# Optimization experiments

Measured on AMD Instinct MI355X. Metric: run time of the kernel, lower is better.

The kernel has to match this reference:

```python
import jax, jax.numpy as jnp
import numpy as np

B, T, I, H = 128, 512, 256, 256


def _gru_layer(x_seq, Wih, Whh, bih, bhh):
    """One GRU layer, batch_first. x_seq: [B, T, I_l]. Returns (outputs [B,T,H], h_T [B,H]).
    PyTorch gate order: r, z, n; n = tanh(Wn x + bn_i + r * (Un h + bn_h)); h' = (1-z)*n + z*h.
    """
    # Precompute input projections for all timesteps: [B, T, 3H]
    x_proj = jnp.einsum('bti,gi->btg', x_seq, Wih) + bih
    Wr_h, Wz_h, Wn_h = jnp.split(Whh, 3, axis=0)   # each [H, H]
    br_h, bz_h, bn_h = jnp.split(bhh, 3)

    def step(h, xp):  # h: [B, H], xp: [B, 3H]
        xr, xz, xn = jnp.split(xp, 3, axis=-1)
        r = jax.nn.sigmoid(xr + h @ Wr_h.T + br_h)
        z = jax.nn.sigmoid(xz + h @ Wz_h.T + bz_h)
        n = jnp.tanh(xn + r * (h @ Wn_h.T + bn_h))
        h_new = (1.0 - z) * n + z * h
        return h_new, h_new

    h0 = jnp.zeros((x_seq.shape[0], Whh.shape[1]), dtype=x_seq.dtype)
    hT, outs = jax.lax.scan(step, h0, jnp.swapaxes(x_proj, 0, 1))  # scan over time
    return jnp.swapaxes(outs, 0, 1), hT


def setup_inputs() -> dict:
    key = jax.random.key(0)
    ks = jax.random.split(key, 12)
    s = 1.0 / np.sqrt(H)  # torch GRU/Linear init scale
    u = lambda k, shape: jax.random.uniform(k, shape, jnp.float32, -s, s)
    return {
        'x': jax.random.normal(ks[0], (B, T, I), jnp.float32),
        'Wih0': u(ks[1], (3 * H, I)),
        'Whh0': u(ks[2], (3 * H, H)),
        'bih0': u(ks[3], (3 * H,)),
        'bhh0': u(ks[4], (3 * H,)),
        'Wih1': u(ks[5], (3 * H, H)),
        'Whh1': u(ks[6], (3 * H, H)),
        'bih1': u(ks[7], (3 * H,)),
        'bhh1': u(ks[8], (3 * H,)),
        'Wfc': u(ks[9], (1, H)),
        'bfc': u(ks[10], (1,)),
    }


def reference(x, Wih0, Whh0, bih0, bhh0, Wih1, Whh1, bih1, bhh1, Wfc, bfc):
    out0, _ = _gru_layer(x, Wih0, Whh0, bih0, bhh0)      # layer 0 outputs [B,T,H]
    _, hT1 = _gru_layer(out0, Wih1, Whh1, bih1, bhh1)     # final hidden of layer 1 [B,H]
    y_logit = hT1 @ Wfc.T + bfc                            # [B, 1]
    return jax.nn.sigmoid(y_logit)
```

## Files before the change

### kernel.cpp

```cpp
#include <hip/hip_runtime.h>
#include <hip/hip_bf16.h>
#include <stdint.h>

#define NB 128
#define NT 512
#define NI 256
#define NH 256
#define NG 768

typedef unsigned int u32;
typedef unsigned short u16;
typedef __attribute__((ext_vector_type(8))) short short8;
typedef __attribute__((ext_vector_type(4))) float f32x4;

__device__ __forceinline__ float lo_bf(u32 u){ return __uint_as_float(u << 16); }
__device__ __forceinline__ float hi_bf(u32 u){ return __uint_as_float(u & 0xffff0000u); }
__device__ __forceinline__ u16 f2bf(float f){
  u32 u = __float_as_uint(f);
  u += 0x7fffu + ((u >> 16) & 1u);
  return (u16)(u >> 16);
}
__device__ __forceinline__ u32 pack2(float a, float b){
  return (u32)f2bf(a) | ((u32)f2bf(b) << 16);
}
__device__ __forceinline__ u32 pack_rne(float a, float b){
  u32 ua = __float_as_uint(a), ub = __float_as_uint(b);
  ua += 0x7fffu + ((ua >> 16) & 1u);
  ub += 0x7fffu + ((ub >> 16) & 1u);
  return (ua >> 16) | (ub & 0xffff0000u);
}
__device__ __forceinline__ float sigf(float v){
  return __builtin_amdgcn_rcpf(1.f + __expf(-v));
}
__device__ __forceinline__ float tanhf_(float u){
  float e = __expf(2.f*u);
  return 1.f - 2.f*__builtin_amdgcn_rcpf(e + 1.f);
}
__device__ __forceinline__ void gload_lds16(const void* g, void* l){
  __builtin_amdgcn_global_load_lds((const __attribute__((address_space(1))) void*)g,
                                   (__attribute__((address_space(3))) void*)l, 16, 0, 0);
}

__global__ void convert_kernel(const float* __restrict__ x,
    const float* __restrict__ Wih0, const float* __restrict__ Wih1,
    const float* __restrict__ bih0, const float* __restrict__ bhh0,
    const float* __restrict__ bih1, const float* __restrict__ bhh1,
    u16* __restrict__ xbf, u16* __restrict__ w0bf, u16* __restrict__ w1bf,
    float* __restrict__ bias0, float* __restrict__ bias1)
{
  const int NX4 = NB*NT*NI/4, NW4 = NG*NH/4;
  int gid = blockIdx.x*blockDim.x + threadIdx.x;
  for (int i = gid; i < NX4 + 2*NW4; i += gridDim.x*blockDim.x) {
    const float* s; u16* d; int o;
    if (i < NX4)          { s = x;    d = xbf;  o = i; }
    else if (i < NX4+NW4) { s = Wih0; d = w0bf; o = i - NX4; }
    else                  { s = Wih1; d = w1bf; o = i - NX4 - NW4; }
    float4 v = *(const float4*)(s + (size_t)o*4);
    uint2 pk; pk.x = pack2(v.x, v.y); pk.y = pack2(v.z, v.w);
    *(uint2*)&d[(size_t)o*4] = pk;
  }
  if (gid < NG)            bias0[gid] = bih0[gid] + (gid < 2*NH ? bhh0[gid] : 0.f);
  else if (gid < 2*NG)   { int g = gid - NG; bias1[g] = bih1[g] + (g < 2*NH ? bhh1[g] : 0.f); }
}

__global__ __launch_bounds__(256, 2) void gemm_proj(const u16* __restrict__ A,
    const u16* __restrict__ W, const float* __restrict__ bias, u16* __restrict__ out)
{
  const int mt = blockIdx.x / 24, nt = blockIdx.x % 24;
  __shared__ __align__(16) u16 As[64*256];
  __shared__ __align__(16) u16 Bs[32*256];
  const int tid = threadIdx.x;
  const u16* Ag = A + (size_t)mt*64*256;
  const u16* Wg = W + (size_t)nt*32*256;
  #pragma unroll
  for (int i = 0; i < 8; ++i) {
    int ca = tid + 256*i, row = ca >> 5, sl = ca & 31;
    gload_lds16(Ag + row*256 + ((sl ^ (row&7))<<3), &As[ca<<3]);
  }
  #pragma unroll
  for (int i = 0; i < 4; ++i) {
    int cb = tid + 256*i, row = cb >> 5, sl = cb & 31;
    gload_lds16(Wg + row*256 + ((sl ^ (row&7))<<3), &Bs[cb<<3]);
  }
  __syncthreads();
  const int w = tid >> 6, l = tid & 63, c = l & 15, q = l >> 4;
  f32x4 acc0 = {0.f,0.f,0.f,0.f}, acc1 = acc0;
  const int arow = w*16 + c;
  #pragma unroll
  for (int kb = 0; kb < 8; ++kb) {
    int ks = kb*4 + q;
    short8 af  = *(const short8*)&As[arow*256 + ((ks ^ (arow&7))<<3)];
    short8 bf0 = *(const short8*)&Bs[c*256        + ((ks ^ (c&7))<<3)];
    short8 bf1 = *(const short8*)&Bs[(16+c)*256   + ((ks ^ ((16+c)&7))<<3)];
    acc0 = __builtin_amdgcn_mfma_f32_16x16x32_bf16(af, bf0, acc0, 0,0,0);
    acc1 = __builtin_amdgcn_mfma_f32_16x16x32_bf16(af, bf1, acc1, 0,0,0);
  }
  #pragma unroll
  for (int nf = 0; nf < 2; ++nf) {
    int g = nt*32 + nf*16 + c;
    float bs = bias[g];
    f32x4 av = nf ? acc1 : acc0;
    #pragma unroll
    for (int r = 0; r < 4; ++r) {
      int m = mt*64 + w*16 + q*4 + r;
      out[(size_t)m*NG + g] = f2bf(av[r] + bs);
    }
  }
}

__global__ __launch_bounds__(512, 1) void recur_kernel(
    const u16* __restrict__ xproj,
    const float* __restrict__ Whh,
    const float* __restrict__ bhh,
    u16* __restrict__ outp,
    int write_all)
{
  const int b0 = blockIdx.x * 8;
  const int tid = threadIdx.x;
  const int w = tid >> 6, l = tid & 63, c = l & 15, q = l >> 4;
  const int jh = c >> 3;
  const bool lo8 = (jh == 0);
  const int bb = b0 + (c & 7);
  const int jb = 32*w + jh*16 + q*4;

  __shared__ __align__(16) u16 hfrag[2][8][512];
  for (int i = tid; i < 4096; i += 512) ((u32*)hfrag)[i] = 0u;

  short8 wf[3][2][8];
  #pragma unroll
  for (int g = 0; g < 3; ++g)
    #pragma unroll
    for (int jj = 0; jj < 2; ++jj) {
      const float* src = Whh + ((size_t)(g*NH + 32*w + jj*16 + c))*NI + q*8;
      #pragma unroll
      for (int kb = 0; kb < 8; ++kb) {
        float4 f0 = *(const float4*)(src + kb*32);
        float4 f1 = *(const float4*)(src + kb*32 + 4);
        short8 s;
        s[0]=(short)f2bf(f0.x); s[1]=(short)f2bf(f0.y);
        s[2]=(short)f2bf(f0.z); s[3]=(short)f2bf(f0.w);
        s[4]=(short)f2bf(f1.x); s[5]=(short)f2bf(f1.y);
        s[6]=(short)f2bf(f1.z); s[7]=(short)f2bf(f1.w);
        wf[g][jj][kb] = s;
      }
    }

  float4 bt0 = *(const float4*)&bhh[2*NH + 32*w + q*4];
  float4 bt1 = *(const float4*)&bhh[2*NH + 32*w + q*4 + 16];
  f32x4 bhn0; bhn0[0]=bt0.x; bhn0[1]=bt0.y; bhn0[2]=bt0.z; bhn0[3]=bt0.w;
  f32x4 bhn1; bhn1[0]=bt1.x; bhn1[1]=bt1.y; bhn1[2]=bt1.z; bhn1[3]=bt1.w;

  const u16* xptr = xproj + (size_t)bb*NT*NG + jb;
  uint2 xpr = *(const uint2*)(xptr);
  uint2 xpz = *(const uint2*)(xptr + NH);
  uint2 xpn = *(const uint2*)(xptr + 2*NH);
  uint2 hpk; hpk.x = 0u; hpk.y = 0u;

  const int lp = (c & 7) + 16*(2*jh + (q >> 1));
  __syncthreads();

  #pragma unroll 1
  for (int t = 0; t < NT; ++t) {
    const int cur = t & 1, nxt = cur ^ 1;

    short8 bfr[8];
    #pragma unroll
    for (int kb = 0; kb < 8; ++kb) bfr[kb] = *(const short8*)&hfrag[cur][kb][l*8];

    const u16* xnx = xptr + (size_t)((t+1 < NT) ? t+1 : t)*NG;
    uint2 nxr = *(const uint2*)(xnx);
    uint2 nxz = *(const uint2*)(xnx + NH);
    uint2 nxn = *(const uint2*)(xnx + 2*NH);

    f32x4 z4 = {0.f,0.f,0.f,0.f};
    f32x4 ar0 = z4, az0 = z4, ar1 = z4, az1 = z4;
    f32x4 an0 = bhn0, an1 = bhn1;
    #pragma unroll
    for (int kb = 0; kb < 8; ++kb) {
      short8 bv = bfr[kb];
      ar0 = __builtin_amdgcn_mfma_f32_16x16x32_bf16(wf[0][0][kb], bv, ar0, 0,0,0);
      az0 = __builtin_amdgcn_mfma_f32_16x16x32_bf16(wf[1][0][kb], bv, az0, 0,0,0);
      an0 = __builtin_amdgcn_mfma_f32_16x16x32_bf16(wf[2][0][kb], bv, an0, 0,0,0);
      ar1 = __builtin_amdgcn_mfma_f32_16x16x32_bf16(wf[0][1][kb], bv, ar1, 0,0,0);
      az1 = __builtin_amdgcn_mfma_f32_16x16x32_bf16(wf[1][1][kb], bv, az1, 0,0,0);
      an1 = __builtin_amdgcn_mfma_f32_16x16x32_bf16(wf[2][1][kb], bv, an1, 0,0,0);
    }

    float hv[4];
    #pragma unroll
    for (int r = 0; r < 4; ++r) {
      float arv = lo8 ? ar0[r] : ar1[r];
      float azv = lo8 ? az0[r] : az1[r];
      float anv = lo8 ? an0[r] : an1[r];
      u32 xrw = (r < 2) ? xpr.x : xpr.y;
      u32 xzw = (r < 2) ? xpz.x : xpz.y;
      u32 xnw = (r < 2) ? xpn.x : xpn.y;
      u32 hpw = (r < 2) ? hpk.x : hpk.y;
      float xr = (r & 1) ? hi_bf(xrw) : lo_bf(xrw);
      float xz = (r & 1) ? hi_bf(xzw) : lo_bf(xzw);
      float xn = (r & 1) ? hi_bf(xnw) : lo_bf(xnw);
      float hp = (r & 1) ? hi_bf(hpw) : lo_bf(hpw);
      float rr = sigf(xr + arv);
      float zz = sigf(xz + azv);
      float nn = tanhf_(__builtin_fmaf(rr, anv, xn));
      hv[r] = __builtin_fmaf(zz, hp - nn, nn);
    }
    hpk.x = pack_rne(hv[0], hv[1]);
    hpk.y = pack_rne(hv[2], hv[3]);

    u16* hdst = &hfrag[nxt][w][lp*8 + (q & 1)*4];
    *(uint2*)hdst        = hpk;
    *(uint2*)(hdst + 64) = hpk;
    if (write_all)
      *(uint2*)&outp[((size_t)bb*NT + t)*NH + jb] = hpk;
    else if (t == NT-1)
      *(uint2*)&outp[(size_t)bb*NH + jb] = hpk;

    xpr = nxr; xpz = nxz; xpn = nxn;
    __syncthreads();
  }
}

__global__ __launch_bounds__(256) void fc_kernel(const u16* __restrict__ hT,
    const float* __restrict__ Wfc, const float* __restrict__ bfc, float* __restrict__ out)
{
  __shared__ float wv[NH];
  int tid = threadIdx.x;
  if (tid < NH) wv[tid] = Wfc[tid];
  __syncthreads();
  if (tid < NB) {
    float acc = bfc[0];
    for (int j = 0; j < NH; ++j) acc += lo_bf((u32)hT[tid*NH + j]) * wv[j];
    out[tid] = sigf(acc);
  }
}

extern "C" void kernel_launch(void* const* d_in, const int* in_sizes, int n_in,
                              void* d_out, int out_size, void* d_ws, size_t ws_size,
                              hipStream_t stream) {
  const float* x    = (const float*)d_in[0];
  const float* Wih0 = (const float*)d_in[1];
  const float* Whh0 = (const float*)d_in[2];
  const float* bih0 = (const float*)d_in[3];
  const float* bhh0 = (const float*)d_in[4];
  const float* Wih1 = (const float*)d_in[5];
  const float* Whh1 = (const float*)d_in[6];
  const float* bih1 = (const float*)d_in[7];
  const float* bhh1 = (const float*)d_in[8];
  const float* Wfc  = (const float*)d_in[9];
  const float* bfc  = (const float*)d_in[10];

  char* ws = (char*)d_ws;
  u16*   xproj = (u16*)ws;
  u16*   xbf   = (u16*)(ws + 100663296);
  u16*   out0  = xbf;
  u16*   w0bf  = (u16*)(ws + 134217728);
  u16*   w1bf  = (u16*)(ws + 134610944);
  float* bias0 = (float*)(ws + 135004160);
  float* bias1 = (float*)(ws + 135007232);
  u16*   hT    = (u16*)(ws + 135010304);

  convert_kernel<<<dim3(2048), dim3(256), 0, stream>>>(
      x, Wih0, Wih1, bih0, bhh0, bih1, bhh1, xbf, w0bf, w1bf, bias0, bias1);
  gemm_proj<<<dim3(1024*24), dim3(256), 0, stream>>>(xbf, w0bf, bias0, xproj);
  recur_kernel<<<dim3(16), dim3(512), 0, stream>>>(xproj, Whh0, bhh0, out0, 1);
  gemm_proj<<<dim3(1024*24), dim3(256), 0, stream>>>(out0, w1bf, bias1, xproj);
  recur_kernel<<<dim3(16), dim3(512), 0, stream>>>(xproj, Whh1, bhh1, hT, 0);
  fc_kernel<<<dim3(1), dim3(256), 0, stream>>>(hT, Wfc, bfc, (float*)d_out);
}
```

Before: 1.399 ms.

## Pipeline both GRU layers and layer-1 input projection in one persistent kernel

Replaces the sequential layer-0 recurrence, layer-1 projection GEMM and layer-1 recurrence with one 48-block kernel split into three roles per batch group. The roles stream results through ring-buffer FIFOs in global memory, using agent-scope atomic counters for flow control. The aim is to overlap the two recurrences in a wavefront pipeline, so the second serial 512-step loop mostly hides behind the first. It also drops the full out0 write and the second large GEMM. The cost is spin-wait synchronisation latency on every step, a dependence on all 48 blocks being co-resident, and a per-timestep Wih1 matvec done on only 16 blocks.

```diff
diff --git a/kernel.cpp b/kernel.cpp
--- a/kernel.cpp
+++ b/kernel.cpp
@@ -7,8 +7,11 @@
 #define NI 256
 #define NH 256
 #define NG 768
+#define NGRP 16
+#define RING 32
 
 typedef unsigned int u32;
+typedef unsigned long long u64;
 typedef unsigned short u16;
 typedef __attribute__((ext_vector_type(8))) short short8;
 typedef __attribute__((ext_vector_type(4))) float f32x4;
@@ -29,6 +32,10 @@
   ub += 0x7fffu + ((ub >> 16) & 1u);
   return (ua >> 16) | (ub & 0xffff0000u);
 }
+__device__ __forceinline__ u64 pack4(const f32x4& v){
+  u32 a = pack_rne(v[0], v[1]), b = pack_rne(v[2], v[3]);
+  return (u64)a | ((u64)b << 32);
+}
 __device__ __forceinline__ float sigf(float v){
   return __builtin_amdgcn_rcpf(1.f + __expf(-v));
 }
@@ -40,27 +47,57 @@
   __builtin_amdgcn_global_load_lds((const __attribute__((address_space(1))) void*)g,
                                    (__attribute__((address_space(3))) void*)l, 16, 0, 0);
 }
+__device__ __forceinline__ void st_agent(u64* p, u64 v){
+  __hip_atomic_store(p, v, __ATOMIC_RELAXED, __HIP_MEMORY_SCOPE_AGENT);
+}
+__device__ __forceinline__ u64 ld_agent(const u64* p){
+  return __hip_atomic_load(p, __ATOMIC_RELAXED, __HIP_MEMORY_SCOPE_AGENT);
+}
+__device__ __forceinline__ u32 spin_ge(u32* p, u32 target, u32 shadow){
+  while (shadow < target) {
+    shadow = __hip_atomic_load(p, __ATOMIC_ACQUIRE, __HIP_MEMORY_SCOPE_AGENT);
+    if (shadow >= target) break;
+    __builtin_amdgcn_s_sleep(2);
+  }
+  return shadow;
+}
+__device__ __forceinline__ void load_frags(const float* W, int w, int c, int q,
+                                           short8 wf[3][2][8]){
+  #pragma unroll
+  for (int g = 0; g < 3; ++g)
+    #pragma unroll
+    for (int jj = 0; jj < 2; ++jj) {
+      const float* src = W + ((size_t)(g*NH + 32*w + jj*16 + c))*NI + q*8;
+      #pragma unroll
+      for (int kb = 0; kb < 8; ++kb) {
+        float4 f0 = *(const float4*)(src + kb*32);
+        float4 f1 = *(const float4*)(src + kb*32 + 4);
+        short8 s;
+        s[0]=(short)f2bf(f0.x); s[1]=(short)f2bf(f0.y);
+        s[2]=(short)f2bf(f0.z); s[3]=(short)f2bf(f0.w);
+        s[4]=(short)f2bf(f1.x); s[5]=(short)f2bf(f1.y);
+        s[6]=(short)f2bf(f1.z); s[7]=(short)f2bf(f1.w);
+        wf[g][jj][kb] = s;
+      }
+    }
+}
 
 __global__ void convert_kernel(const float* __restrict__ x,
-    const float* __restrict__ Wih0, const float* __restrict__ Wih1,
+    const float* __restrict__ Wih0,
     const float* __restrict__ bih0, const float* __restrict__ bhh0,
-    const float* __restrict__ bih1, const float* __restrict__ bhh1,
-    u16* __restrict__ xbf, u16* __restrict__ w0bf, u16* __restrict__ w1bf,
-    float* __restrict__ bias0, float* __restrict__ bias1)
+    u16* __restrict__ xbf, u16* __restrict__ w0bf, float* __restrict__ bias0)
 {
   const int NX4 = NB*NT*NI/4, NW4 = NG*NH/4;
   int gid = blockIdx.x*blockDim.x + threadIdx.x;
-  for (int i = gid; i < NX4 + 2*NW4; i += gridDim.x*blockDim.x) {
+  for (int i = gid; i < NX4 + NW4; i += gridDim.x*blockDim.x) {
     const float* s; u16* d; int o;
-    if (i < NX4)          { s = x;    d = xbf;  o = i; }
-    else if (i < NX4+NW4) { s = Wih0; d = w0bf; o = i - NX4; }
-    else                  { s = Wih1; d = w1bf; o = i - NX4 - NW4; }
+    if (i < NX4) { s = x;    d = xbf;  o = i; }
+    else         { s = Wih0; d = w0bf; o = i - NX4; }
     float4 v = *(const float4*)(s + (size_t)o*4);
     uint2 pk; pk.x = pack2(v.x, v.y); pk.y = pack2(v.z, v.w);
     *(uint2*)&d[(size_t)o*4] = pk;
   }
-  if (gid < NG)            bias0[gid] = bih0[gid] + (gid < 2*NH ? bhh0[gid] : 0.f);
-  else if (gid < 2*NG)   { int g = gid - NG; bias1[g] = bih1[g] + (g < 2*NH ? bhh1[g] : 0.f); }
+  if (gid < NG) bias0[gid] = bih0[gid] + (gid < 2*NH ? bhh0[gid] : 0.f);
 }
 
 __global__ __launch_bounds__(256, 2) void gemm_proj(const u16* __restrict__ A,
@@ -108,116 +145,284 @@
   }
 }
 
-__global__ __launch_bounds__(512, 1) void recur_kernel(
-    const u16* __restrict__ xproj,
-    const float* __restrict__ Whh,
-    const float* __restrict__ bhh,
-    u16* __restrict__ outp,
-    int write_all)
+__global__ __launch_bounds__(512, 1) void pipeline_kernel(
+    const u16*  __restrict__ xproj,
+    const float* __restrict__ Whh0, const float* __restrict__ bhh0,
+    const float* __restrict__ Wih1, const float* __restrict__ bih1,
+    const float* __restrict__ bhh1, const float* __restrict__ Whh1,
+    u16* __restrict__ hT,
+    u16* __restrict__ fifo_h0,
+    u16* __restrict__ fifo_xp,
+    u32* __restrict__ cnts)
 {
-  const int b0 = blockIdx.x * 8;
+  const int role = blockIdx.x >> 4;
+  const int g_   = blockIdx.x & 15;
+  const int b0   = g_*8;
   const int tid = threadIdx.x;
   const int w = tid >> 6, l = tid & 63, c = l & 15, q = l >> 4;
-  const int jh = c >> 3;
-  const bool lo8 = (jh == 0);
-  const int bb = b0 + (c & 7);
-  const int jb = 32*w + jh*16 + q*4;
+
+  u32* cntA = cnts + (0*NGRP + g_)*32;
+  u32* cntB = cnts + (1*NGRP + g_)*32;
+  u32* cntC = cnts + (2*NGRP + g_)*32;
+  u16* slots_h0 = fifo_h0 + (size_t)g_*RING*4096;
+  u16* slots_xp = fifo_xp + (size_t)g_*RING*8*NG;
 
   __shared__ __align__(16) u16 hfrag[2][8][512];
   for (int i = tid; i < 4096; i += 512) ((u32*)hfrag)[i] = 0u;
-
-  short8 wf[3][2][8];
-  #pragma unroll
-  for (int g = 0; g < 3; ++g)
+  __syncthreads();
+
+  if (role == 0) {
+    short8 wf[3][2][8];
+    load_frags(Whh0, w, c, q, wf);
+    float4 bt0 = *(const float4*)&bhh0[2*NH + 32*w + q*4];
+    float4 bt1 = *(const float4*)&bhh0[2*NH + 32*w + q*4 + 16];
+    f32x4 bhn0; bhn0[0]=bt0.x; bhn0[1]=bt0.y; bhn0[2]=bt0.z; bhn0[3]=bt0.w;
+    f32x4 bhn1; bhn1[0]=bt1.x; bhn1[1]=bt1.y; bhn1[2]=bt1.z; bhn1[3]=bt1.w;
+    const int jh = c >> 3;
+    const bool lo8 = (jh == 0);
+    const int bb = b0 + (c & 7);
+    const int jb = 32*w + jh*16 + q*4;
+    const u16* xptr = xproj + (size_t)bb*NT*NG + jb;
+    uint2 xpr = *(const uint2*)(xptr);
+    uint2 xpz = *(const uint2*)(xptr + NH);
+    uint2 xpn = *(const uint2*)(xptr + 2*NH);
+    const u16* x1 = xptr + NG;
+    uint2 pfr = *(const uint2*)(x1);
+    uint2 pfz = *(const uint2*)(x1 + NH);
+    uint2 pfn = *(const uint2*)(x1 + 2*NH);
+    uint2 hpk; hpk.x = 0u; hpk.y = 0u;
+    const int lp = (c&7) + 16*(2*jh + (q>>1));
+    const int foff = w*512 + lp*8 + (q&1)*4;
+    u32 shadowB = 0;
+
+    #pragma unroll 1
+    for (int t = 0; t < NT; ++t) {
+      const int cur = t & 1, nxt = cur ^ 1;
+      short8 bfr[8];
+      #pragma unroll
+      for (int kb = 0; kb < 8; ++kb) bfr[kb] = *(const short8*)&hfrag[cur][kb][l*8];
+      f32x4 z4 = {0.f,0.f,0.f,0.f};
+      f32x4 ar0 = z4, az0 = z4, ar1 = z4, az1 = z4;
+      f32x4 an0 = bhn0, an1 = bhn1;
+      #pragma unroll
+      for (int kb = 0; kb < 8; ++kb) {
+        short8 bv = bfr[kb];
+        ar0 = __builtin_amdgcn_mfma_f32_16x16x32_bf16(wf[0][0][kb], bv, ar0, 0,0,0);
+        az0 = __builtin_amdgcn_mfma_f32_16x16x32_bf16(wf[1][0][kb], bv, az0, 0,0,0);
+        an0 = __builtin_amdgcn_mfma_f32_16x16x32_bf16(wf[2][0][kb], bv, an0, 0,0,0);
+        ar1 = __builtin_amdgcn_mfma_f32_16x16x32_bf16(wf[0][1][kb], bv, ar1, 0,0,0);
+        az1 = __builtin_amdgcn_mfma_f32_16x16x32_bf16(wf[1][1][kb], bv, az1, 0,0,0);
+        an1 = __builtin_amdgcn_mfma_f32_16x16x32_bf16(wf[2][1][kb], bv, an1, 0,0,0);
+      }
+      float hv[4];
+      #pragma unroll
+      for (int r = 0; r < 4; ++r) {
+        float arv = lo8 ? ar0[r] : ar1[r];
+        float azv = lo8 ? az0[r] : az1[r];
+        float anv = lo8 ? an0[r] : an1[r];
+        u32 xrw = (r < 2) ? xpr.x : xpr.y;
+        u32 xzw = (r < 2) ? xpz.x : xpz.y;
+        u32 xnw = (r < 2) ? xpn.x : xpn.y;
+        u32 hpw = (r < 2) ? hpk.x : hpk.y;
+        float xr = (r & 1) ? hi_bf(xrw) : lo_bf(xrw);
+        float xz = (r & 1) ? hi_bf(xzw) : lo_bf(xzw);
+        float xn = (r & 1) ? hi_bf(xnw) : lo_bf(xnw);
+        float hp = (r & 1) ? hi_bf(hpw) : lo_bf(hpw);
+        float rr = sigf(xr + arv);
+        float zz = sigf(xz + azv);
+        float nn = tanhf_(__builtin_fmaf(rr, anv, xn));
+        hv[r] = __builtin_fmaf(zz, hp - nn, nn);
+      }
+      hpk.x = pack_rne(hv[0], hv[1]);
+      hpk.y = pack_rne(hv[2], hv[3]);
+
+      u16* hdst = &hfrag[nxt][w][lp*8 + (q&1)*4];
+      *(uint2*)hdst        = hpk;
+      *(uint2*)(hdst + 64) = hpk;
+
+      if (t >= 29) {
+        u32 tgt = 8u*(u32)(t - 28);
+        if (shadowB < tgt) shadowB = spin_ge(cntB, tgt, shadowB);
+      }
+      u64 hv64 = (u64)hpk.x | ((u64)hpk.y << 32);
+      u16* sb = slots_h0 + (size_t)(t & (RING-1))*4096 + foff;
+      st_agent((u64*)sb, hv64);
+      st_agent((u64*)(sb + 64), hv64);
+      if (l == 0)
+        __hip_atomic_fetch_add(cntA, 1u, __ATOMIC_RELEASE, __HIP_MEMORY_SCOPE_AGENT);
+
+      xpr = pfr; xpz = pfz; xpn = pfn;
+      if (t + 2 < NT) {
+        const u16* xn_ = xptr + (size_t)(t+2)*NG;
+        pfr = *(const uint2*)(xn_);
+        pfz = *(const uint2*)(xn_ + NH);
+        pfn = *(const uint2*)(xn_ + 2*NH);
+      }
+      asm volatile("s_waitcnt lgkmcnt(0)" ::: "memory");
+      __builtin_amdgcn_s_barrier();
+      __builtin_amdgcn_sched_barrier(0);
+    }
+
+  } else if (role == 1) {
+    short8 wf[3][2][8];
+    load_frags(Wih1, w, c, q, wf);
+    f32x4 bias[3][2];
     #pragma unroll
-    for (int jj = 0; jj < 2; ++jj) {
-      const float* src = Whh + ((size_t)(g*NH + 32*w + jj*16 + c))*NI + q*8;
+    for (int g = 0; g < 3; ++g)
+      #pragma unroll
+      for (int jj = 0; jj < 2; ++jj) {
+        int grow = g*NH + 32*w + jj*16 + q*4;
+        float4 bi = *(const float4*)&bih1[grow];
+        f32x4 bv; bv[0]=bi.x; bv[1]=bi.y; bv[2]=bi.z; bv[3]=bi.w;
+        if (g < 2) {
+          float4 bh = *(const float4*)&bhh1[grow];
+          bv[0]+=bh.x; bv[1]+=bh.y; bv[2]+=bh.z; bv[3]+=bh.w;
+        }
+        bias[g][jj] = bv;
+      }
+    const int jj = c >> 3;
+    u32 shadowA = 0, shadowC = 0;
+    shadowA = spin_ge(cntA, 8u, shadowA);
+    const u16* s0 = slots_h0 + 0*4096 + tid*8;
+    u64 wc0 = ld_agent((const u64*)s0), wc1 = ld_agent((const u64*)(s0 + 4));
+    shadowA = spin_ge(cntA, 16u, shadowA);
+    const u16* s1 = slots_h0 + 1*4096 + tid*8;
+    u64 pf0 = ld_agent((const u64*)s1), pf1 = ld_agent((const u64*)(s1 + 4));
+
+    #pragma unroll 1
+    for (int t = 0; t < NT; ++t) {
+      const int buf = t & 1;
+      uint4 wv; wv.x=(u32)wc0; wv.y=(u32)(wc0>>32); wv.z=(u32)wc1; wv.w=(u32)(wc1>>32);
+      *(uint4*)&((u16*)hfrag)[buf*4096 + tid*8] = wv;
+      asm volatile("s_waitcnt lgkmcnt(0)" ::: "memory");
+      __builtin_amdgcn_s_barrier();
+      __builtin_amdgcn_sched_barrier(0);
+
+      f32x4 a00 = bias[0][0], a10 = bias[1][0], a20 = bias[2][0];
+      f32x4 a01 = bias[0][1], a11 = bias[1][1], a21 = bias[2][1];
       #pragma unroll
       for (int kb = 0; kb < 8; ++kb) {
-        float4 f0 = *(const float4*)(src + kb*32);
-        float4 f1 = *(const float4*)(src + kb*32 + 4);
-        short8 s;
-        s[0]=(short)f2bf(f0.x); s[1]=(short)f2bf(f0.y);
-        s[2]=(short)f2bf(f0.z); s[3]=(short)f2bf(f0.w);
-        s[4]=(short)f2bf(f1.x); s[5]=(short)f2bf(f1.y);
-        s[6]=(short)f2bf(f1.z); s[7]=(short)f2bf(f1.w);
-        wf[g][jj][kb] = s;
+        short8 bv = *(const short8*)&hfrag[buf][kb][l*8];
+        a00 = __builtin_amdgcn_mfma_f32_16x16x32_bf16(wf[0][0][kb], bv, a00, 0,0,0);
+        a10 = __builtin_amdgcn_mfma_f32_16x16x32_bf16(wf[1][0][kb], bv, a10, 0,0,0);
+        a20 = __builtin_amdgcn_mfma_f32_16x16x32_bf16(wf[2][0][kb], bv, a20, 0,0,0);
+        a01 = __builtin_amdgcn_mfma_f32_16x16x32_bf16(wf[0][1][kb], bv, a01, 0,0,0);
+        a11 = __builtin_amdgcn_mfma_f32_16x16x32_bf16(wf[1][1][kb], bv, a11, 0,0,0);
+        a21 = __builtin_amdgcn_mfma_f32_16x16x32_bf16(wf[2][1][kb], bv, a21, 0,0,0);
+      }
+      f32x4 v0 = jj ? a01 : a00, v1 = jj ? a11 : a10, v2 = jj ? a21 : a20;
+      if (t >= 29) {
+        u32 tgt = 8u*(u32)(t - 28);
+        if (shadowC < tgt) shadowC = spin_ge(cntC, tgt, shadowC);
+      }
+      u16* xb_ = slots_xp + (size_t)(t & (RING-1))*8*NG
+               + (size_t)(c & 7)*NG + 32*w + jj*16 + q*4;
+      st_agent((u64*)(xb_),        pack4(v0));
+      st_agent((u64*)(xb_ + NH),   pack4(v1));
+      st_agent((u64*)(xb_ + 2*NH), pack4(v2));
+      if (l == 0)
+        __hip_atomic_fetch_add(cntB, 1u, __ATOMIC_RELEASE, __HIP_MEMORY_SCOPE_AGENT);
+      wc0 = pf0; wc1 = pf1;
+      if (t + 2 < NT) {
+        u32 tgt = 8u*(u32)(t + 3);
+        if (shadowA < tgt) shadowA = spin_ge(cntA, tgt, shadowA);
+        const u16* sn = slots_h0 + (size_t)((t+2) & (RING-1))*4096 + tid*8;
+        pf0 = ld_agent((const u64*)sn); pf1 = ld_agent((const u64*)(sn + 4));
       }
     }
 
-  float4 bt0 = *(const float4*)&bhh[2*NH + 32*w + q*4];
-  float4 bt1 = *(const float4*)&bhh[2*NH + 32*w + q*4 + 16];
-  f32x4 bhn0; bhn0[0]=bt0.x; bhn0[1]=bt0.y; bhn0[2]=bt0.z; bhn0[3]=bt0.w;
-  f32x4 bhn1; bhn1[0]=bt1.x; bhn1[1]=bt1.y; bhn1[2]=bt1.z; bhn1[3]=bt1.w;
-
-  const u16* xptr = xproj + (size_t)bb*NT*NG + jb;
-  uint2 xpr = *(const uint2*)(xptr);
-  uint2 xpz = *(const uint2*)(xptr + NH);
-  uint2 xpn = *(const uint2*)(xptr + 2*NH);
-  uint2 hpk; hpk.x = 0u; hpk.y = 0u;
-
-  const int lp = (c & 7) + 16*(2*jh + (q >> 1));
-  __syncthreads();
-
-  #pragma unroll 1
-  for (int t = 0; t < NT; ++t) {
-    const int cur = t & 1, nxt = cur ^ 1;
-
-    short8 bfr[8];
-    #pragma unroll
-    for (int kb = 0; kb < 8; ++kb) bfr[kb] = *(const short8*)&hfrag[cur][kb][l*8];
-
-    const u16* xnx = xptr + (size_t)((t+1 < NT) ? t+1 : t)*NG;
-    uint2 nxr = *(const uint2*)(xnx);
-    uint2 nxz = *(const uint2*)(xnx + NH);
-    uint2 nxn = *(const uint2*)(xnx + 2*NH);
-
-    f32x4 z4 = {0.f,0.f,0.f,0.f};
-    f32x4 ar0 = z4, az0 = z4, ar1 = z4, az1 = z4;
-    f32x4 an0 = bhn0, an1 = bhn1;
-    #pragma unroll
-    for (int kb = 0; kb < 8; ++kb) {
-      short8 bv = bfr[kb];
-      ar0 = __builtin_amdgcn_mfma_f32_16x16x32_bf16(wf[0][0][kb], bv, ar0, 0,0,0);
-      az0 = __builtin_amdgcn_mfma_f32_16x16x32_bf16(wf[1][0][kb], bv, az0, 0,0,0);
-      an0 = __builtin_amdgcn_mfma_f32_16x16x32_bf16(wf[2][0][kb], bv, an0, 0,0,0);
-      ar1 = __builtin_amdgcn_mfma_f32_16x16x32_bf16(wf[0][1][kb], bv, ar1, 0,0,0);
-      az1 = __builtin_amdgcn_mfma_f32_16x16x32_bf16(wf[1][1][kb], bv, az1, 0,0,0);
-      an1 = __builtin_amdgcn_mfma_f32_16x16x32_bf16(wf[2][1][kb], bv, an1, 0,0,0);
+  } else {
+    short8 wf[3][2][8];
+    load_frags(Whh1, w, c, q, wf);
+    float4 bt0 = *(const float4*)&bhh1[2*NH + 32*w + q*4];
+    float4 bt1 = *(const float4*)&bhh1[2*NH + 32*w + q*4 + 16];
+    f32x4 bhn0; bhn0[0]=bt0.x; bhn0[1]=bt0.y; bhn0[2]=bt0.z; bhn0[3]=bt0.w;
+    f32x4 bhn1; bhn1[0]=bt1.x; bhn1[1]=bt1.y; bhn1[2]=bt1.z; bhn1[3]=bt1.w;
+    const int jh = c >> 3;
+    const bool lo8 = (jh == 0);
+    const int bb = b0 + (c & 7);
+    const int jb = 32*w + jh*16 + q*4;
+    const int lp = (c&7) + 16*(2*jh + (q>>1));
+    const size_t xoff = (size_t)(c & 7)*NG + jb;
+    u32 shadowB = 0;
+    shadowB = spin_ge(cntB, 8u, shadowB);
+    u64 vr = ld_agent((const u64*)(slots_xp + xoff));
+    u64 vz = ld_agent((const u64*)(slots_xp + xoff + NH));
+    u64 vn = ld_agent((const u64*)(slots_xp + xoff + 2*NH));
+    uint2 xpr, xpz, xpn;
+    xpr.x=(u32)vr; xpr.y=(u32)(vr>>32);
+    xpz.x=(u32)vz; xpz.y=(u32)(vz>>32);
+    xpn.x=(u32)vn; xpn.y=(u32)(vn>>32);
+    shadowB = spin_ge(cntB, 16u, shadowB);
+    u64 pr = ld_agent((const u64*)(slots_xp + 1*8*NG + xoff));
+    u64 pz = ld_agent((const u64*)(slots_xp + 1*8*NG + xoff + NH));
+    u64 pn = ld_agent((const u64*)(slots_xp + 1*8*NG + xoff + 2*NH));
+    uint2 hpk; hpk.x = 0u; hpk.y = 0u;
+
+    #pragma unroll 1
+    for (int t = 0; t < NT; ++t) {
+      const int cur = t & 1, nxt = cur ^ 1;
+      short8 bfr[8];
+      #pragma unroll
+      for (int kb = 0; kb < 8; ++kb) bfr[kb] = *(const short8*)&hfrag[cur][kb][l*8];
+      f32x4 z4 = {0.f,0.f,0.f,0.f};
+      f32x4 ar0 = z4, az0 = z4, ar1 = z4, az1 = z4;
+      f32x4 an0 = bhn0, an1 = bhn1;
+      #pragma unroll
+      for (int kb = 0; kb < 8; ++kb) {
+        short8 bv = bfr[kb];
+        ar0 = __builtin_amdgcn_mfma_f32_16x16x32_bf16(wf[0][0][kb], bv, ar0, 0,0,0);
+        az0 = __builtin_amdgcn_mfma_f32_16x16x32_bf16(wf[1][0][kb], bv, az0, 0,0,0);
+        an0 = __builtin_amdgcn_mfma_f32_16x16x32_bf16(wf[2][0][kb], bv, an0, 0,0,0);
+        ar1 = __builtin_amdgcn_mfma_f32_16x16x32_bf16(wf[0][1][kb], bv, ar1, 0,0,0);
+        az1 = __builtin_amdgcn_mfma_f32_16x16x32_bf16(wf[1][1][kb], bv, az1, 0,0,0);
+        an1 = __builtin_amdgcn_mfma_f32_16x16x32_bf16(wf[2][1][kb], bv, an1, 0,0,0);
+      }
+      float hv[4];
+      #pragma unroll
+      for (int r = 0; r < 4; ++r) {
+        float arv = lo8 ? ar0[r] : ar1[r];
+        float azv = lo8 ? az0[r] : az1[r];
+        float anv = lo8 ? an0[r] : an1[r];
+        u32 xrw = (r < 2) ? xpr.x : xpr.y;
+        u32 xzw = (r < 2) ? xpz.x : xpz.y;
+        u32 xnw = (r < 2) ? xpn.x : xpn.y;
+        u32 hpw = (r < 2) ? hpk.x : hpk.y;
+        float xr = (r & 1) ? hi_bf(xrw) : lo_bf(xrw);
+        float xz = (r & 1) ? hi_bf(xzw) : lo_bf(xzw);
+        float xn = (r & 1) ? hi_bf(xnw) : lo_bf(xnw);
+        float hp = (r & 1) ? hi_bf(hpw) : lo_bf(hpw);
+        float rr = sigf(xr + arv);
+        float zz = sigf(xz + azv);
+        float nn = tanhf_(__builtin_fmaf(rr, anv, xn));
+        hv[r] = __builtin_fmaf(zz, hp - nn, nn);
+      }
+      hpk.x = pack_rne(hv[0], hv[1]);
+      hpk.y = pack_rne(hv[2], hv[3]);
+
+      u16* hdst = &hfrag[nxt][w][lp*8 + (q&1)*4];
+      *(uint2*)hdst        = hpk;
+      *(uint2*)(hdst + 64) = hpk;
+      if (t == NT-1)
+        *(uint2*)&hT[(size_t)bb*NH + jb] = hpk;
+      if (l == 0)
+        __hip_atomic_fetch_add(cntC, 1u, __ATOMIC_RELEASE, __HIP_MEMORY_SCOPE_AGENT);
+
+      xpr.x=(u32)pr; xpr.y=(u32)(pr>>32);
+      xpz.x=(u32)pz; xpz.y=(u32)(pz>>32);
+      xpn.x=(u32)pn; xpn.y=(u32)(pn>>32);
+      if (t + 2 < NT) {
+        u32 tgt = 8u*(u32)(t + 3);
+        if (shadowB < tgt) shadowB = spin_ge(cntB, tgt, shadowB);
+        const u16* sn = slots_xp + (size_t)((t+2) & (RING-1))*8*NG + xoff;
+        pr = ld_agent((const u64*)(sn));
+        pz = ld_agent((const u64*)(sn + NH));
+        pn = ld_agent((const u64*)(sn + 2*NH));
+      }
+      asm volatile("s_waitcnt lgkmcnt(0)" ::: "memory");
+      __builtin_amdgcn_s_barrier();
+      __builtin_amdgcn_sched_barrier(0);
     }
-
-    float hv[4];
-    #pragma unroll
-    for (int r = 0; r < 4; ++r) {
-      float arv = lo8 ? ar0[r] : ar1[r];
-      float azv = lo8 ? az0[r] : az1[r];
-      float anv = lo8 ? an0[r] : an1[r];
-      u32 xrw = (r < 2) ? xpr.x : xpr.y;
-      u32 xzw = (r < 2) ? xpz.x : xpz.y;
-      u32 xnw = (r < 2) ? xpn.x : xpn.y;
-      u32 hpw = (r < 2) ? hpk.x : hpk.y;
-      float xr = (r & 1) ? hi_bf(xrw) : lo_bf(xrw);
-      float xz = (r & 1) ? hi_bf(xzw) : lo_bf(xzw);
-      float xn = (r & 1) ? hi_bf(xnw) : lo_bf(xnw);
-      float hp = (r & 1) ? hi_bf(hpw) : lo_bf(hpw);
-      float rr = sigf(xr + arv);
-      float zz = sigf(xz + azv);
-      float nn = tanhf_(__builtin_fmaf(rr, anv, xn));
-      hv[r] = __builtin_fmaf(zz, hp - nn, nn);
-    }
-    hpk.x = pack_rne(hv[0], hv[1]);
-    hpk.y = pack_rne(hv[2], hv[3]);
-
-    u16* hdst = &hfrag[nxt][w][lp*8 + (q & 1)*4];
-    *(uint2*)hdst        = hpk;
-    *(uint2*)(hdst + 64) = hpk;
-    if (write_all)
-      *(uint2*)&outp[((size_t)bb*NT + t)*NH + jb] = hpk;
-    else if (t == NT-1)
-      *(uint2*)&outp[(size_t)bb*NH + jb] = hpk;
-
-    xpr = nxr; xpz = nxz; xpn = nxn;
-    __syncthreads();
   }
 }
 
@@ -251,20 +456,20 @@
   const float* bfc  = (const float*)d_in[10];
 
   char* ws = (char*)d_ws;
-  u16*   xproj = (u16*)ws;
-  u16*   xbf   = (u16*)(ws + 100663296);
-  u16*   out0  = xbf;
-  u16*   w0bf  = (u16*)(ws + 134217728);
-  u16*   w1bf  = (u16*)(ws + 134610944);
-  float* bias0 = (float*)(ws + 135004160);
-  float* bias1 = (float*)(ws + 135007232);
-  u16*   hT    = (u16*)(ws + 135010304);
+  u16*   xproj   = (u16*)ws;
+  u16*   xbf     = (u16*)(ws + 100663296);
+  u16*   fifo_h0 = (u16*)(ws + 100663296);
+  u16*   fifo_xp = (u16*)(ws + 100663296 + 4194304);
+  u32*   cnts    = (u32*)(ws + 100663296 + 4194304 + 6291456);
+  u16*   w0bf    = (u16*)(ws + 134217728);
+  float* bias0   = (float*)(ws + 135004160);
+  u16*   hT      = (u16*)(ws + 135010304);
 
   convert_kernel<<<dim3(2048), dim3(256), 0, stream>>>(
-      x, Wih0, Wih1, bih0, bhh0, bih1, bhh1, xbf, w0bf, w1bf, bias0, bias1);
+      x, Wih0, bih0, bhh0, xbf, w0bf, bias0);
   gemm_proj<<<dim3(1024*24), dim3(256), 0, stream>>>(xbf, w0bf, bias0, xproj);
-  recur_kernel<<<dim3(16), dim3(512), 0, stream>>>(xproj, Whh0, bhh0, out0, 1);
-  gemm_proj<<<dim3(1024*24), dim3(256), 0, stream>>>(out0, w1bf, bias1, xproj);
-  recur_kernel<<<dim3(16), dim3(512), 0, stream>>>(xproj, Whh1, bhh1, hT, 0);
+  hipMemsetAsync(cnts, 0, 3*NGRP*32*sizeof(u32), stream);
+  pipeline_kernel<<<dim3(48), dim3(512), 0, stream>>>(
+      xproj, Whh0, bhh0, Wih1, bih1, bhh1, Whh1, hT, fifo_h0, fifo_xp, cnts);
   fc_kernel<<<dim3(1), dim3(256), 0, stream>>>(hT, Wfc, bfc, (float*)d_out);
 }
```

New measurement: 3.318 ms. +137.1%, slower.

## Split recurrence over twice as many blocks with four batch rows each

Applied to the files above, without the earlier changes.

Each recurrent block now handles 4 batch rows instead of 8, so the grid doubles from 16 to 32 blocks and each lane finishes 2 hidden outputs instead of 4. The hidden-state fragment is replicated four times in LDS to fill the 16-wide MFMA column dimension, so half the MFMA columns do redundant work. The input-projection prefetch now runs two steps ahead. Priority is raised around the MFMA loop, and the per-step __syncthreads is replaced by an explicit lgkm wait plus a raw barrier. The aim is to shorten the serial per-step elementwise tail and use more CUs, at the cost of wasted matrix throughput.

```diff
diff --git a/kernel.cpp b/kernel.cpp
--- a/kernel.cpp
+++ b/kernel.cpp
@@ -115,13 +115,15 @@
     u16* __restrict__ outp,
     int write_all)
 {
-  const int b0 = blockIdx.x * 8;
+  const int b0 = blockIdx.x * 4;
   const int tid = threadIdx.x;
   const int w = tid >> 6, l = tid & 63, c = l & 15, q = l >> 4;
   const int jh = c >> 3;
+  const int rs = (c >> 2) & 1;
   const bool lo8 = (jh == 0);
-  const int bb = b0 + (c & 7);
-  const int jb = 32*w + jh*16 + q*4;
+  const bool rlo = (rs == 0);
+  const int bb = b0 + (c & 3);
+  const int j0 = 32*w + jh*16 + q*4 + 2*rs;
 
   __shared__ __align__(16) u16 hfrag[2][8][512];
   for (int i = tid; i < 4096; i += 512) ((u32*)hfrag)[i] = 0u;
@@ -150,13 +152,20 @@
   f32x4 bhn0; bhn0[0]=bt0.x; bhn0[1]=bt0.y; bhn0[2]=bt0.z; bhn0[3]=bt0.w;
   f32x4 bhn1; bhn1[0]=bt1.x; bhn1[1]=bt1.y; bhn1[2]=bt1.z; bhn1[3]=bt1.w;
 
-  const u16* xptr = xproj + (size_t)bb*NT*NG + jb;
-  uint2 xpr = *(const uint2*)(xptr);
-  uint2 xpz = *(const uint2*)(xptr + NH);
-  uint2 xpn = *(const uint2*)(xptr + 2*NH);
-  uint2 hpk; hpk.x = 0u; hpk.y = 0u;
-
-  const int lp = (c & 7) + 16*(2*jh + (q >> 1));
+  const u16* xptr = xproj + (size_t)bb*NT*NG + j0;
+  u32 xpr = *(const u32*)(xptr);
+  u32 xpz = *(const u32*)(xptr + NH);
+  u32 xpn = *(const u32*)(xptr + 2*NH);
+  const u16* x1 = xptr + NG;
+  u32 pfr = *(const u32*)(x1);
+  u32 pfz = *(const u32*)(x1 + NH);
+  u32 pfn = *(const u32*)(x1 + 2*NH);
+  u32 hpk = 0u;
+
+  const int lpb  = (c & 3) + 16*(2*jh + (q >> 1));
+  const int elds = 4*(q & 1) + 2*rs;
+  const int woff = lpb*8 + elds;
+
   __syncthreads();
 
   #pragma unroll 1
@@ -167,14 +176,10 @@
     #pragma unroll
     for (int kb = 0; kb < 8; ++kb) bfr[kb] = *(const short8*)&hfrag[cur][kb][l*8];
 
-    const u16* xnx = xptr + (size_t)((t+1 < NT) ? t+1 : t)*NG;
-    uint2 nxr = *(const uint2*)(xnx);
-    uint2 nxz = *(const uint2*)(xnx + NH);
-    uint2 nxn = *(const uint2*)(xnx + 2*NH);
-
     f32x4 z4 = {0.f,0.f,0.f,0.f};
     f32x4 ar0 = z4, az0 = z4, ar1 = z4, az1 = z4;
     f32x4 an0 = bhn0, an1 = bhn1;
+    __builtin_amdgcn_s_setprio(1);
     #pragma unroll
     for (int kb = 0; kb < 8; ++kb) {
       short8 bv = bfr[kb];
@@ -185,39 +190,53 @@
       az1 = __builtin_amdgcn_mfma_f32_16x16x32_bf16(wf[1][1][kb], bv, az1, 0,0,0);
       an1 = __builtin_amdgcn_mfma_f32_16x16x32_bf16(wf[2][1][kb], bv, an1, 0,0,0);
     }
-
-    float hv[4];
-    #pragma unroll
-    for (int r = 0; r < 4; ++r) {
-      float arv = lo8 ? ar0[r] : ar1[r];
-      float azv = lo8 ? az0[r] : az1[r];
-      float anv = lo8 ? an0[r] : an1[r];
-      u32 xrw = (r < 2) ? xpr.x : xpr.y;
-      u32 xzw = (r < 2) ? xpz.x : xpz.y;
-      u32 xnw = (r < 2) ? xpn.x : xpn.y;
-      u32 hpw = (r < 2) ? hpk.x : hpk.y;
-      float xr = (r & 1) ? hi_bf(xrw) : lo_bf(xrw);
-      float xz = (r & 1) ? hi_bf(xzw) : lo_bf(xzw);
-      float xn = (r & 1) ? hi_bf(xnw) : lo_bf(xnw);
-      float hp = (r & 1) ? hi_bf(hpw) : lo_bf(hpw);
+    __builtin_amdgcn_s_setprio(0);
+
+    float hv[2];
+    #pragma unroll
+    for (int e = 0; e < 2; ++e) {
+      float a0 = rlo ? ar0[e] : ar0[2+e];
+      float a1 = rlo ? ar1[e] : ar1[2+e];
+      float arv = lo8 ? a0 : a1;
+      float z0 = rlo ? az0[e] : az0[2+e];
+      float z1 = rlo ? az1[e] : az1[2+e];
+      float azv = lo8 ? z0 : z1;
+      float n0 = rlo ? an0[e] : an0[2+e];
+      float n1 = rlo ? an1[e] : an1[2+e];
+      float anv = lo8 ? n0 : n1;
+      float xr = e ? hi_bf(xpr) : lo_bf(xpr);
+      float xz = e ? hi_bf(xpz) : lo_bf(xpz);
+      float xn = e ? hi_bf(xpn) : lo_bf(xpn);
+      float hp = e ? hi_bf(hpk) : lo_bf(hpk);
       float rr = sigf(xr + arv);
       float zz = sigf(xz + azv);
       float nn = tanhf_(__builtin_fmaf(rr, anv, xn));
-      hv[r] = __builtin_fmaf(zz, hp - nn, nn);
-    }
-    hpk.x = pack_rne(hv[0], hv[1]);
-    hpk.y = pack_rne(hv[2], hv[3]);
-
-    u16* hdst = &hfrag[nxt][w][lp*8 + (q & 1)*4];
-    *(uint2*)hdst        = hpk;
-    *(uint2*)(hdst + 64) = hpk;
+      hv[e] = __builtin_fmaf(zz, hp - nn, nn);
+    }
+    hpk = pack_rne(hv[0], hv[1]);
+
+    u16* hd = &hfrag[nxt][w][woff];
+    *(u32*)(hd)       = hpk;
+    *(u32*)(hd + 32)  = hpk;
+    *(u32*)(hd + 64)  = hpk;
+    *(u32*)(hd + 96)  = hpk;
+
     if (write_all)
-      *(uint2*)&outp[((size_t)bb*NT + t)*NH + jb] = hpk;
+      *(u32*)&outp[((size_t)bb*NT + t)*NH + j0] = hpk;
     else if (t == NT-1)
-      *(uint2*)&outp[(size_t)bb*NH + jb] = hpk;
-
-    xpr = nxr; xpz = nxz; xpn = nxn;
-    __syncthreads();
+      *(u32*)&outp[(size_t)bb*NH + j0] = hpk;
+
+    xpr = pfr; xpz = pfz; xpn = pfn;
+    if (t + 2 < NT) {
+      const u16* xn_ = xptr + (size_t)(t+2)*NG;
+      pfr = *(const u32*)(xn_);
+      pfz = *(const u32*)(xn_ + NH);
+      pfn = *(const u32*)(xn_ + 2*NH);
+    }
+
+    asm volatile("s_waitcnt lgkmcnt(0)" ::: "memory");
+    __builtin_amdgcn_s_barrier();
+    __builtin_amdgcn_sched_barrier(0);
   }
 }
 
@@ -263,8 +282,8 @@
   convert_kernel<<<dim3(2048), dim3(256), 0, stream>>>(
       x, Wih0, Wih1, bih0, bhh0, bih1, bhh1, xbf, w0bf, w1bf, bias0, bias1);
   gemm_proj<<<dim3(1024*24), dim3(256), 0, stream>>>(xbf, w0bf, bias0, xproj);
-  recur_kernel<<<dim3(16), dim3(512), 0, stream>>>(xproj, Whh0, bhh0, out0, 1);
+  recur_kernel<<<dim3(32), dim3(512), 0, stream>>>(xproj, Whh0, bhh0, out0, 1);
   gemm_proj<<<dim3(1024*24), dim3(256), 0, stream>>>(out0, w1bf, bias1, xproj);
-  recur_kernel<<<dim3(16), dim3(512), 0, stream>>>(xproj, Whh1, bhh1, hT, 0);
+  recur_kernel<<<dim3(32), dim3(512), 0, stream>>>(xproj, Whh1, bhh1, hT, 0);
   fc_kernel<<<dim3(1), dim3(256), 0, stream>>>(hT, Wfc, bfc, (float*)d_out);
 }
```

New measurement: 2.066 ms. 1.48x slower.

## Fuse fp32-to-bf16 input conversion into layer-0 projection GEMM and relax barrier

Applied to the files above, without the earlier changes.

The separate conversion pass over x to bf16 is removed. The layer-0 projection GEMM now reads fp32 x directly and packs it to bf16 while staging it into shared memory, which avoids writing and re-reading a 64 MB bf16 copy. Each of the 24 N-tiles now re-reads the fp32 A tile, twice the bytes of the bf16 copy, and the load goes through registers instead of direct global-to-LDS loads. The recurrence loop's __syncthreads is also replaced by an explicit lgkmcnt wait plus s_barrier, which skips waiting on outstanding global stores.

```diff
diff --git a/kernel.cpp b/kernel.cpp
--- a/kernel.cpp
+++ b/kernel.cpp
@@ -41,20 +41,19 @@
                                    (__attribute__((address_space(3))) void*)l, 16, 0, 0);
 }
 
-__global__ void convert_kernel(const float* __restrict__ x,
+__global__ void convert_kernel(
     const float* __restrict__ Wih0, const float* __restrict__ Wih1,
     const float* __restrict__ bih0, const float* __restrict__ bhh0,
     const float* __restrict__ bih1, const float* __restrict__ bhh1,
-    u16* __restrict__ xbf, u16* __restrict__ w0bf, u16* __restrict__ w1bf,
+    u16* __restrict__ w0bf, u16* __restrict__ w1bf,
     float* __restrict__ bias0, float* __restrict__ bias1)
 {
-  const int NX4 = NB*NT*NI/4, NW4 = NG*NH/4;
+  const int NW4 = NG*NH/4;
   int gid = blockIdx.x*blockDim.x + threadIdx.x;
-  for (int i = gid; i < NX4 + 2*NW4; i += gridDim.x*blockDim.x) {
+  for (int i = gid; i < 2*NW4; i += gridDim.x*blockDim.x) {
     const float* s; u16* d; int o;
-    if (i < NX4)          { s = x;    d = xbf;  o = i; }
-    else if (i < NX4+NW4) { s = Wih0; d = w0bf; o = i - NX4; }
-    else                  { s = Wih1; d = w1bf; o = i - NX4 - NW4; }
+    if (i < NW4) { s = Wih0; d = w0bf; o = i; }
+    else         { s = Wih1; d = w1bf; o = i - NW4; }
     float4 v = *(const float4*)(s + (size_t)o*4);
     uint2 pk; pk.x = pack2(v.x, v.y); pk.y = pack2(v.z, v.w);
     *(uint2*)&d[(size_t)o*4] = pk;
@@ -63,23 +62,35 @@
   else if (gid < 2*NG)   { int g = gid - NG; bias1[g] = bih1[g] + (g < 2*NH ? bhh1[g] : 0.f); }
 }
 
-__global__ __launch_bounds__(256, 2) void gemm_proj(const u16* __restrict__ A,
+template <bool A_F32>
+__global__ __launch_bounds__(256, 2) void gemm_proj(const void* __restrict__ Ap,
     const u16* __restrict__ W, const float* __restrict__ bias, u16* __restrict__ out)
 {
   const int mt = blockIdx.x / 24, nt = blockIdx.x % 24;
   __shared__ __align__(16) u16 As[64*256];
   __shared__ __align__(16) u16 Bs[32*256];
   const int tid = threadIdx.x;
-  const u16* Ag = A + (size_t)mt*64*256;
-  const u16* Wg = W + (size_t)nt*32*256;
   #pragma unroll
   for (int i = 0; i < 8; ++i) {
     int ca = tid + 256*i, row = ca >> 5, sl = ca & 31;
-    gload_lds16(Ag + row*256 + ((sl ^ (row&7))<<3), &As[ca<<3]);
+    if (A_F32) {
+      const float* Ag = (const float*)Ap + (size_t)mt*64*256;
+      const float* src = Ag + row*256 + sl*8;
+      float4 f0 = *(const float4*)(src);
+      float4 f1 = *(const float4*)(src + 4);
+      uint4 pk;
+      pk.x = pack2(f0.x, f0.y); pk.y = pack2(f0.z, f0.w);
+      pk.z = pack2(f1.x, f1.y); pk.w = pack2(f1.z, f1.w);
+      *(uint4*)&As[(row<<8) + ((sl ^ (row&7))<<3)] = pk;
+    } else {
+      const u16* Ag = (const u16*)Ap + (size_t)mt*64*256;
+      gload_lds16(Ag + row*256 + ((sl ^ (row&7))<<3), &As[ca<<3]);
+    }
   }
   #pragma unroll
   for (int i = 0; i < 4; ++i) {
     int cb = tid + 256*i, row = cb >> 5, sl = cb & 31;
+    const u16* Wg = W + (size_t)nt*32*256;
     gload_lds16(Wg + row*256 + ((sl ^ (row&7))<<3), &Bs[cb<<3]);
   }
   __syncthreads();
@@ -217,7 +228,10 @@
       *(uint2*)&outp[(size_t)bb*NH + jb] = hpk;
 
     xpr = nxr; xpz = nxz; xpn = nxn;
-    __syncthreads();
+
+    asm volatile("s_waitcnt lgkmcnt(0)" ::: "memory");
+    __builtin_amdgcn_s_barrier();
+    __builtin_amdgcn_sched_barrier(0);
   }
 }
 
@@ -252,19 +266,18 @@
 
   char* ws = (char*)d_ws;
   u16*   xproj = (u16*)ws;
-  u16*   xbf   = (u16*)(ws + 100663296);
-  u16*   out0  = xbf;
+  u16*   out0  = (u16*)(ws + 100663296);
   u16*   w0bf  = (u16*)(ws + 134217728);
   u16*   w1bf  = (u16*)(ws + 134610944);
   float* bias0 = (float*)(ws + 135004160);
   float* bias1 = (float*)(ws + 135007232);
   u16*   hT    = (u16*)(ws + 135010304);
 
-  convert_kernel<<<dim3(2048), dim3(256), 0, stream>>>(
-      x, Wih0, Wih1, bih0, bhh0, bih1, bhh1, xbf, w0bf, w1bf, bias0, bias1);
-  gemm_proj<<<dim3(1024*24), dim3(256), 0, stream>>>(xbf, w0bf, bias0, xproj);
+  convert_kernel<<<dim3(512), dim3(256), 0, stream>>>(
+      Wih0, Wih1, bih0, bhh0, bih1, bhh1, w0bf, w1bf, bias0, bias1);
+  gemm_proj<true ><<<dim3(1024*24), dim3(256), 0, stream>>>(x,    w0bf, bias0, xproj);
   recur_kernel<<<dim3(16), dim3(512), 0, stream>>>(xproj, Whh0, bhh0, out0, 1);
-  gemm_proj<<<dim3(1024*24), dim3(256), 0, stream>>>(out0, w1bf, bias1, xproj);
+  gemm_proj<false><<<dim3(1024*24), dim3(256), 0, stream>>>(out0, w1bf, bias1, xproj);
   recur_kernel<<<dim3(16), dim3(512), 0, stream>>>(xproj, Whh1, bhh1, hT, 0);
   fc_kernel<<<dim3(1), dim3(256), 0, stream>>>(hT, Wfc, bfc, (float*)d_out);
 }
```

Measured after the change: 1.421 ms. No clear change (+1.6%).
